# Optimization experiments

Measured on AMD Instinct MI355X. Metric: run time of the kernel, lower is better.

The kernel has to match this reference:

```python
import jax, jax.numpy as jnp
import numpy as np

ATTEN_SIZE = 16
HIDDEN = 512


def setup_inputs() -> dict:
    key = jax.random.key(0)
    ks = jax.random.split(key, 6)
    B, S, D_in, H, D_out = 64, 100, 256, HIDDEN, 256
    # xavier-normal-ish scale for weights
    def xav(k, shape):
        fan_in, fan_out = shape
        std = np.sqrt(2.0 / (fan_in + fan_out))
        return jax.random.normal(k, shape, dtype=jnp.float32) * std
    return {
        "x": jax.random.normal(ks[0], (B, S, D_in), dtype=jnp.float32),
        "W0": xav(ks[1], (D_in, H)),
        "b0": jnp.zeros((1, 1, H), dtype=jnp.float32),
        "Wq": xav(ks[2], (H, H)),
        "Wk": xav(ks[3], (H, H)),
        "Wv": xav(ks[4], (H, H)),
        "W1": xav(ks[5], (H, D_out)),
        "b1": jnp.zeros((1, 1, D_out), dtype=jnp.float32),
    }


def reference(x, W0, b0, Wq, Wk, Wv, W1, b1):
    w = ATTEN_SIZE
    win = 2 * w + 1
    B, S = x.shape[0], x.shape[1]
    # pre-attention MLP layer (atten_layer_index = 1)
    h = jax.nn.relu(x @ W0 + b0)  # [B, S, H]
    # sliding-window neighbor gather, matching pad + roll(k) + stack + slice:
    # x_nei[:, i, k_idx] = padded[:, i + 2w - k_idx]  (reversed window order)
    padded = jnp.pad(h, ((0, 0), (w, w), (0, 0)))  # [B, S+2w, H]
    idx = jnp.arange(S)[:, None] + (2 * w - jnp.arange(win))[None, :]
    x_nei = padded[:, idx]
    q = x_nei @ Wq
    k = x_nei @ Wk
    v = x_nei @ Wv
    d = jnp.einsum('bswh,buh_->bswu'.replace('h_', 'sh'[1] + 'h'), q, k) if False else jnp.einsum('bswh,bsuh->bswu', q, k)
    d = d / jnp.sqrt(jnp.float32(HIDDEN))
    alpha = jax.nn.softmax(d, axis=-1)
    wv = jnp.einsum('bswu,bsuh->bswh', alpha, v)
    out = wv.sum(axis=2)  # sum over window rows -> [B, S, H]
    y = jax.nn.relu(out @ W1 + b1)  # [B, S, D_out]
    return y, alpha.reshape(B * S, win, win)
```

## Files before the change

kernel.cpp:

```cpp
#include <hip/hip_runtime.h>

typedef __bf16 bf16x8 __attribute__((ext_vector_type(8)));
typedef float f32x4 __attribute__((ext_vector_type(4)));
typedef unsigned int u32;

__device__ __forceinline__ unsigned short f2bf(float f) {
  unsigned int u = __float_as_uint(f);
  u += 0x7FFFu + ((u >> 16) & 1u);
  return (unsigned short)(u >> 16);
}
__device__ __forceinline__ float bf2f(unsigned short s) {
  return __uint_as_float(((unsigned int)s) << 16);
}

__device__ __forceinline__ void gload16(const void* g, void* l) {
  __builtin_amdgcn_global_load_lds(
      (const __attribute__((address_space(1))) u32*)g,
      (__attribute__((address_space(3))) u32*)l, 16, 0, 0);
}

__global__ __launch_bounds__(256) void prep_kernel(
    const float* __restrict__ x, const float* __restrict__ W0,
    const float* __restrict__ Wq, const float* __restrict__ Wk,
    const float* __restrict__ Wv, const float* __restrict__ W1,
    unsigned short* __restrict__ xb, unsigned short* __restrict__ w0t,
    unsigned short* __restrict__ wqkvt, unsigned short* __restrict__ w1t)
{
  __shared__ float tile[32][33];
  const int bid = blockIdx.x, tid = threadIdx.x;
  if (bid < 1600) {
    long i = (long)bid * 1024 + tid * 4;
    float4 v = *(const float4*)(x + i);
    unsigned short o0 = f2bf(v.x), o1 = f2bf(v.y), o2 = f2bf(v.z), o3 = f2bf(v.w);
    ushort4 o = {o0, o1, o2, o3};
    *(ushort4*)(xb + i) = o;
    return;
  }
  int id = bid - 1600;
  const float* src; unsigned short* dst;
  int N, DLD, k0, n0, drow0;
  if (id < 128) {
    src = W0; N = 512; dst = w0t; DLD = 256;
    k0 = (id >> 4) * 32; n0 = (id & 15) * 32; drow0 = n0;
  } else if (id < 896) {
    int id1 = id - 128, which = id1 >> 8, rem = id1 & 255;
    src = (which == 0) ? Wq : (which == 1) ? Wk : Wv;
    N = 512; dst = wqkvt; DLD = 512;
    k0 = (rem >> 4) * 32; n0 = (rem & 15) * 32; drow0 = which * 512 + n0;
  } else {
    int id2 = id - 896;
    src = W1; N = 256; dst = w1t; DLD = 512;
    k0 = (id2 >> 3) * 32; n0 = (id2 & 7) * 32; drow0 = n0;
  }
  const int tr = tid >> 5, tc = tid & 31;
#pragma unroll
  for (int rr = 0; rr < 4; ++rr) {
    int kl = tr + rr * 8;
    tile[kl][tc] = src[(long)(k0 + kl) * N + n0 + tc];
  }
  __syncthreads();
#pragma unroll
  for (int rr = 0; rr < 4; ++rr) {
    int nl = tr + rr * 8;
    dst[(long)(drow0 + nl) * DLD + k0 + tc] = f2bf(tile[tc][nl]);
  }
}

template<bool RELU, bool OUT_BF16>
__global__ __launch_bounds__(256) void gemm_tile(
    const unsigned short* __restrict__ A, int lda,
    const unsigned short* __restrict__ Bt, int ldb,
    const float* __restrict__ bias,
    void* __restrict__ Cout, int ldc, int KT)
{
  __shared__ unsigned short As[2][64 * 32];
  __shared__ unsigned short Bs[2][128 * 32];
  const int tid = threadIdx.x;
  const int m0 = blockIdx.x * 64;
  const int n0 = blockIdx.y * 128;
  const int w = tid >> 6, lane = tid & 63;
  const int lr = lane & 15, kq = lane >> 4;

  const unsigned short* Ag  = A  + (long)(m0 + (tid >> 2)) * lda + (tid & 3) * 8;
  const unsigned short* Bg0 = Bt + (long)(n0 + (tid >> 2)) * ldb + (tid & 3) * 8;
  const unsigned short* Bg1 = Bg0 + (long)64 * ldb;

  f32x4 acc[4][2];
#pragma unroll
  for (int i = 0; i < 4; i++)
#pragma unroll
    for (int j = 0; j < 2; j++) acc[i][j] = (f32x4){0.f, 0.f, 0.f, 0.f};

#define STAGE(buf, kt) do { int ko = (kt) * 32;                      \
    gload16(Ag + ko,  &As[buf][tid * 8]);                            \
    gload16(Bg0 + ko, &Bs[buf][tid * 8]);                            \
    gload16(Bg1 + ko, &Bs[buf][(tid + 256) * 8]); } while (0)

  STAGE(0, 0);
  __syncthreads();
  int cur = 0;
  for (int kt = 0; kt < KT; ++kt) {
    if (kt + 1 < KT) STAGE(cur ^ 1, kt + 1);
    bf16x8 af[4], bfr[2];
#pragma unroll
    for (int ii = 0; ii < 4; ii++)
      af[ii] = *(const bf16x8*)&As[cur][(16 * ii + lr) * 32 + 8 * kq];
#pragma unroll
    for (int jj = 0; jj < 2; jj++)
      bfr[jj] = *(const bf16x8*)&Bs[cur][(w * 32 + 16 * jj + lr) * 32 + 8 * kq];
#pragma unroll
    for (int ii = 0; ii < 4; ii++)
#pragma unroll
      for (int jj = 0; jj < 2; jj++)
        acc[ii][jj] = __builtin_amdgcn_mfma_f32_16x16x32_bf16(af[ii], bfr[jj], acc[ii][jj], 0, 0, 0);
    __syncthreads();
    cur ^= 1;
  }
#undef STAGE

#pragma unroll
  for (int ii = 0; ii < 4; ii++) {
#pragma unroll
    for (int jj = 0; jj < 2; jj++) {
      int col = n0 + w * 32 + 16 * jj + lr;
      float bv = bias ? bias[col] : 0.0f;
#pragma unroll
      for (int r = 0; r < 4; r++) {
        int row = m0 + 16 * ii + 4 * kq + r;
        float v = acc[ii][jj][r] + bv;
        if (RELU) v = fmaxf(v, 0.0f);
        if (OUT_BF16) ((unsigned short*)Cout)[(long)row * ldc + col] = f2bf(v);
        else          ((float*)Cout)[(long)row * ldc + col] = v;
      }
    }
  }
}

__global__ __launch_bounds__(256) void gram_tile(
    const unsigned short* __restrict__ qkv, float* __restrict__ G)
{
  const float scale = 0.044194173824159216f;
  __shared__ unsigned short As[2][64 * 32];
  __shared__ unsigned short Bs[2][128 * 32];
  const int tid = threadIdx.x;
  const int m0 = blockIdx.x * 64;
  const int b  = blockIdx.y;
  const int w = tid >> 6, lane = tid & 63;
  const int lr = lane & 15, kq = lane >> 4;

  const unsigned short* A  = qkv + (long)b * 100 * 1536;
  const unsigned short* Bt = A + 512;
  const unsigned short* Ag  = A  + (long)(m0 + (tid >> 2)) * 1536 + (tid & 3) * 8;
  const unsigned short* Bg0 = Bt + (long)(tid >> 2) * 1536 + (tid & 3) * 8;
  const unsigned short* Bg1 = Bg0 + (long)64 * 1536;

  f32x4 acc[4][2];
#pragma unroll
  for (int i = 0; i < 4; i++)
#pragma unroll
    for (int j = 0; j < 2; j++) acc[i][j] = (f32x4){0.f, 0.f, 0.f, 0.f};

#define STAGE(buf, kt) do { int ko = (kt) * 32;                      \
    gload16(Ag + ko,  &As[buf][tid * 8]);                            \
    gload16(Bg0 + ko, &Bs[buf][tid * 8]);                            \
    gload16(Bg1 + ko, &Bs[buf][(tid + 256) * 8]); } while (0)

  STAGE(0, 0);
  __syncthreads();
  int cur = 0;
  for (int kt = 0; kt < 16; ++kt) {
    if (kt + 1 < 16) STAGE(cur ^ 1, kt + 1);
    bf16x8 af[4], bfr[2];
#pragma unroll
    for (int ii = 0; ii < 4; ii++)
      af[ii] = *(const bf16x8*)&As[cur][(16 * ii + lr) * 32 + 8 * kq];
#pragma unroll
    for (int jj = 0; jj < 2; jj++)
      bfr[jj] = *(const bf16x8*)&Bs[cur][(w * 32 + 16 * jj + lr) * 32 + 8 * kq];
#pragma unroll
    for (int ii = 0; ii < 4; ii++)
#pragma unroll
      for (int jj = 0; jj < 2; jj++)
        acc[ii][jj] = __builtin_amdgcn_mfma_f32_16x16x32_bf16(af[ii], bfr[jj], acc[ii][jj], 0, 0, 0);
    __syncthreads();
    cur ^= 1;
  }
#undef STAGE

  float* Gb = G + (long)b * 10000;
#pragma unroll
  for (int ii = 0; ii < 4; ii++) {
#pragma unroll
    for (int jj = 0; jj < 2; jj++) {
      int j = w * 32 + 16 * jj + lr;
#pragma unroll
      for (int r = 0; r < 4; r++) {
        int i = m0 + 16 * ii + 4 * kq + r;
        if (i < 100 && j < 100) Gb[i * 100 + j] = acc[ii][jj][r] * scale;
      }
    }
  }
}

__global__ __launch_bounds__(256) void attn_kernel(
    const float* __restrict__ G,
    const unsigned short* __restrict__ qkv,
    float* __restrict__ alpha_out,
    unsigned short* __restrict__ outb)
{
  const int blk = blockIdx.x;
  const int b = blk / 100, s = blk % 100;
  __shared__ float dmat[33][36];
  __shared__ float rowmax[33], rowinv[33];
  __shared__ float beta[36];
  const int tid = threadIdx.x;
  const float* Gb = G + (long)b * 10000;

  for (int t = tid; t < 1089; t += 256) {
    int dw = t / 33, du = t % 33;
    int i = s + 16 - dw, j = s + 16 - du;
    float v = 0.f;
    if ((unsigned)i < 100u && (unsigned)j < 100u) v = Gb[i * 100 + j];
    dmat[dw][du] = v;
  }
  __syncthreads();

  if (tid < 132) {
    int row = tid >> 2, g = tid & 3;
    float m = -1e30f;
    for (int u = g; u < 33; u += 4) m = fmaxf(m, dmat[row][u]);
    m = fmaxf(m, __shfl_xor(m, 1));
    m = fmaxf(m, __shfl_xor(m, 2));
    float ssum = 0.f;
    for (int u = g; u < 33; u += 4) ssum += __expf(dmat[row][u] - m);
    ssum += __shfl_xor(ssum, 1);
    ssum += __shfl_xor(ssum, 2);
    if (g == 0) { rowmax[row] = m; rowinv[row] = 1.0f / ssum; }
  }
  __syncthreads();

  float* aout = alpha_out + (long)blk * 1089;
  for (int t = tid; t < 1089; t += 256) {
    int dw = t / 33, du = t % 33;
    float a = __expf(dmat[dw][du] - rowmax[dw]) * rowinv[dw];
    aout[t] = a;
    dmat[dw][du] = a;
  }
  __syncthreads();

  if (tid < 33) {
    float sum = 0.f;
    for (int w = 0; w < 33; ++w) sum += dmat[w][tid];
    beta[tid] = sum;
  }
  __syncthreads();

  const unsigned short* vbase = qkv + (long)(b * 100) * 1536 + 1024;
  {
    int c = tid;
    float acc0 = 0.f, acc1 = 0.f;
    for (int u = 0; u < 33; ++u) {
      int p = s + 16 - u;
      if ((unsigned)p < 100u) {
        float bw = beta[u];
        const unsigned short* vr = vbase + (long)p * 1536;
        acc0 += bw * bf2f(vr[c]);
        acc1 += bw * bf2f(vr[c + 256]);
      }
    }
    unsigned short* orow = outb + (long)blk * 512;
    orow[c]       = f2bf(acc0);
    orow[c + 256] = f2bf(acc1);
  }
}

extern "C" void kernel_launch(void* const* d_in, const int* in_sizes, int n_in,
                              void* d_out, int out_size, void* d_ws, size_t ws_size,
                              hipStream_t stream) {
  const float* x  = (const float*)d_in[0];
  const float* W0 = (const float*)d_in[1];
  const float* b0 = (const float*)d_in[2];
  const float* Wq = (const float*)d_in[3];
  const float* Wk = (const float*)d_in[4];
  const float* Wv = (const float*)d_in[5];
  const float* W1 = (const float*)d_in[6];
  const float* b1 = (const float*)d_in[7];

  char* ws = (char*)d_ws;
  unsigned short* xb    = (unsigned short*)(ws + 0);
  unsigned short* w0t   = (unsigned short*)(ws + 3276800);
  unsigned short* wqkvt = (unsigned short*)(ws + 3538944);
  unsigned short* w1t   = (unsigned short*)(ws + 5111808);
  unsigned short* h     = (unsigned short*)(ws + 5373952);
  unsigned short* qkv   = (unsigned short*)(ws + 11927552);
  float*          G     = (float*)(ws + 31686656);
  unsigned short* outb  = (unsigned short*)(ws + 34246656);

  float* y_out     = (float*)d_out;
  float* alpha_out = y_out + 6400 * 256;

  prep_kernel<<<2624, 256, 0, stream>>>(x, W0, Wq, Wk, Wv, W1, xb, w0t, wqkvt, w1t);
  gemm_tile<true,  true ><<<dim3(100, 4),  256, 0, stream>>>(xb, 256, w0t, 256, b0, h, 512, 8);
  gemm_tile<false, true ><<<dim3(100, 12), 256, 0, stream>>>(h, 512, wqkvt, 512, nullptr, qkv, 1536, 16);
  gram_tile<<<dim3(2, 64), 256, 0, stream>>>(qkv, G);
  attn_kernel<<<6400, 256, 0, stream>>>(G, qkv, alpha_out, outb);
  gemm_tile<true,  false><<<dim3(100, 2),  256, 0, stream>>>(outb, 512, w1t, 512, b1, y_out, 256, 16);
}
```

Measured before the change: 178.2 us.

## Swizzle LDS tiles, drop softmax max pass, parallelize beta sum, vectorize V loads

XOR-swizzles the 16-byte chunk index in the LDS tiles of the GEMM and Gram kernels, applied consistently on the global-to-LDS store and the MFMA fragment reads, to reduce LDS bank conflicts. The attention kernel now exponentiates scores directly without subtracting the row max, which removes a reduction pass but risks overflow for large scores. The column sum for beta is spread over 132 threads with shuffle reductions, and the V loads and output stores are packed into 32-bit accesses of two adjacent bf16 values.

```diff
diff --git a/kernel.cpp b/kernel.cpp
--- a/kernel.cpp
+++ b/kernel.cpp
@@ -31,8 +31,7 @@
   if (bid < 1600) {
     long i = (long)bid * 1024 + tid * 4;
     float4 v = *(const float4*)(x + i);
-    unsigned short o0 = f2bf(v.x), o1 = f2bf(v.y), o2 = f2bf(v.z), o3 = f2bf(v.w);
-    ushort4 o = {o0, o1, o2, o3};
+    ushort4 o = {f2bf(v.x), f2bf(v.y), f2bf(v.z), f2bf(v.w)};
     *(ushort4*)(xb + i) = o;
     return;
   }
@@ -80,9 +79,11 @@
   const int n0 = blockIdx.y * 128;
   const int w = tid >> 6, lane = tid & 63;
   const int lr = lane & 15, kq = lane >> 4;
-
-  const unsigned short* Ag  = A  + (long)(m0 + (tid >> 2)) * lda + (tid & 3) * 8;
-  const unsigned short* Bg0 = Bt + (long)(n0 + (tid >> 2)) * ldb + (tid & 3) * 8;
+  const int cg  = (tid & 3) ^ ((tid >> 3) & 3);
+  const int kqs = kq ^ ((lr >> 1) & 3);
+
+  const unsigned short* Ag  = A  + (long)(m0 + (tid >> 2)) * lda + cg * 8;
+  const unsigned short* Bg0 = Bt + (long)(n0 + (tid >> 2)) * ldb + cg * 8;
   const unsigned short* Bg1 = Bg0 + (long)64 * ldb;
 
   f32x4 acc[4][2];
@@ -104,10 +105,10 @@
     bf16x8 af[4], bfr[2];
 #pragma unroll
     for (int ii = 0; ii < 4; ii++)
-      af[ii] = *(const bf16x8*)&As[cur][(16 * ii + lr) * 32 + 8 * kq];
+      af[ii] = *(const bf16x8*)&As[cur][(16 * ii + lr) * 32 + 8 * kqs];
 #pragma unroll
     for (int jj = 0; jj < 2; jj++)
-      bfr[jj] = *(const bf16x8*)&Bs[cur][(w * 32 + 16 * jj + lr) * 32 + 8 * kq];
+      bfr[jj] = *(const bf16x8*)&Bs[cur][(w * 32 + 16 * jj + lr) * 32 + 8 * kqs];
 #pragma unroll
     for (int ii = 0; ii < 4; ii++)
 #pragma unroll
@@ -147,11 +148,13 @@
   const int b  = blockIdx.y;
   const int w = tid >> 6, lane = tid & 63;
   const int lr = lane & 15, kq = lane >> 4;
+  const int cg  = (tid & 3) ^ ((tid >> 3) & 3);
+  const int kqs = kq ^ ((lr >> 1) & 3);
 
   const unsigned short* A  = qkv + (long)b * 100 * 1536;
   const unsigned short* Bt = A + 512;
-  const unsigned short* Ag  = A  + (long)(m0 + (tid >> 2)) * 1536 + (tid & 3) * 8;
-  const unsigned short* Bg0 = Bt + (long)(tid >> 2) * 1536 + (tid & 3) * 8;
+  const unsigned short* Ag  = A  + (long)(m0 + (tid >> 2)) * 1536 + cg * 8;
+  const unsigned short* Bg0 = Bt + (long)(tid >> 2) * 1536 + cg * 8;
   const unsigned short* Bg1 = Bg0 + (long)64 * 1536;
 
   f32x4 acc[4][2];
@@ -173,10 +176,10 @@
     bf16x8 af[4], bfr[2];
 #pragma unroll
     for (int ii = 0; ii < 4; ii++)
-      af[ii] = *(const bf16x8*)&As[cur][(16 * ii + lr) * 32 + 8 * kq];
+      af[ii] = *(const bf16x8*)&As[cur][(16 * ii + lr) * 32 + 8 * kqs];
 #pragma unroll
     for (int jj = 0; jj < 2; jj++)
-      bfr[jj] = *(const bf16x8*)&Bs[cur][(w * 32 + 16 * jj + lr) * 32 + 8 * kq];
+      bfr[jj] = *(const bf16x8*)&Bs[cur][(w * 32 + 16 * jj + lr) * 32 + 8 * kqs];
 #pragma unroll
     for (int ii = 0; ii < 4; ii++)
 #pragma unroll
@@ -211,7 +214,7 @@
   const int blk = blockIdx.x;
   const int b = blk / 100, s = blk % 100;
   __shared__ float dmat[33][36];
-  __shared__ float rowmax[33], rowinv[33];
+  __shared__ float rowinv[33];
   __shared__ float beta[36];
   const int tid = threadIdx.x;
   const float* Gb = G + (long)b * 10000;
@@ -221,56 +224,53 @@
     int i = s + 16 - dw, j = s + 16 - du;
     float v = 0.f;
     if ((unsigned)i < 100u && (unsigned)j < 100u) v = Gb[i * 100 + j];
-    dmat[dw][du] = v;
+    dmat[dw][du] = __expf(v);
   }
   __syncthreads();
 
   if (tid < 132) {
     int row = tid >> 2, g = tid & 3;
-    float m = -1e30f;
-    for (int u = g; u < 33; u += 4) m = fmaxf(m, dmat[row][u]);
-    m = fmaxf(m, __shfl_xor(m, 1));
-    m = fmaxf(m, __shfl_xor(m, 2));
     float ssum = 0.f;
-    for (int u = g; u < 33; u += 4) ssum += __expf(dmat[row][u] - m);
+    for (int u = g; u < 33; u += 4) ssum += dmat[row][u];
     ssum += __shfl_xor(ssum, 1);
     ssum += __shfl_xor(ssum, 2);
-    if (g == 0) { rowmax[row] = m; rowinv[row] = 1.0f / ssum; }
+    if (g == 0) rowinv[row] = 1.0f / ssum;
   }
   __syncthreads();
 
   float* aout = alpha_out + (long)blk * 1089;
   for (int t = tid; t < 1089; t += 256) {
     int dw = t / 33, du = t % 33;
-    float a = __expf(dmat[dw][du] - rowmax[dw]) * rowinv[dw];
+    float a = dmat[dw][du] * rowinv[dw];
     aout[t] = a;
     dmat[dw][du] = a;
   }
   __syncthreads();
 
-  if (tid < 33) {
+  if (tid < 132) {
+    int col = tid >> 2, g = tid & 3;
     float sum = 0.f;
-    for (int w = 0; w < 33; ++w) sum += dmat[w][tid];
-    beta[tid] = sum;
+    for (int w = g; w < 33; w += 4) sum += dmat[w][col];
+    sum += __shfl_xor(sum, 1);
+    sum += __shfl_xor(sum, 2);
+    if (g == 0) beta[col] = sum;
   }
   __syncthreads();
 
   const unsigned short* vbase = qkv + (long)(b * 100) * 1536 + 1024;
   {
-    int c = tid;
     float acc0 = 0.f, acc1 = 0.f;
     for (int u = 0; u < 33; ++u) {
       int p = s + 16 - u;
       if ((unsigned)p < 100u) {
         float bw = beta[u];
-        const unsigned short* vr = vbase + (long)p * 1536;
-        acc0 += bw * bf2f(vr[c]);
-        acc1 += bw * bf2f(vr[c + 256]);
+        u32 pv = *(const u32*)(vbase + (long)p * 1536 + 2 * tid);
+        acc0 += bw * bf2f((unsigned short)(pv & 0xFFFFu));
+        acc1 += bw * bf2f((unsigned short)(pv >> 16));
       }
     }
-    unsigned short* orow = outb + (long)blk * 512;
-    orow[c]       = f2bf(acc0);
-    orow[c + 256] = f2bf(acc1);
+    u32 packed = (u32)f2bf(acc0) | ((u32)f2bf(acc1) << 16);
+    *(u32*)(outb + (long)blk * 512 + 2 * tid) = packed;
   }
 }
 
```

Measured after the change: 176.5 us. Within noise of the previous version (-1.0%).
